# Kernel tuning notes

Measured on AMD Instinct MI355X. Metric: run time of the kernel, lower is better.

## Reference

```python
import jax, jax.numpy as jnp
import numpy as np

ALPHA = 0.2          # LeakyReLU negative slope
NEG = -9.0e15        # masking value from the torch code
B, N, F, O, H = 8, 1024, 256, 128, 8


def setup_inputs() -> dict:
    key = jax.random.key(0)
    ks = jax.random.split(key, 12)
    inputs = jax.random.normal(ks[0], (B, N, F), dtype=jnp.float32)
    adj = jax.random.randint(ks[1], (B, N, N), 0, 2, dtype=jnp.int32)
    mask = jnp.ones((B, N), dtype=jnp.float32)  # unused by forward, kept for signature fidelity
    s = 0.08
    # per-head GAT layers (stacked): W [H,F,O], attention vector a split into src/dst halves
    W_att = jax.random.normal(ks[2], (H, F, O), dtype=jnp.float32) * s
    a_src = jax.random.normal(ks[3], (H, O), dtype=jnp.float32) * s
    a_dst = jax.random.normal(ks[4], (H, O), dtype=jnp.float32) * s
    # output GAT layer: in = H*O, out = O
    W_out = jax.random.normal(ks[5], (H * O, O), dtype=jnp.float32) * s
    ao_src = jax.random.normal(ks[6], (O,), dtype=jnp.float32) * s
    ao_dst = jax.random.normal(ks[7], (O,), dtype=jnp.float32) * s
    # nn.Linear(H*O, O) and nn.Linear(O, O)
    lin_w = jax.random.normal(ks[8], (O, H * O), dtype=jnp.float32) * s
    lin_b = jax.random.normal(ks[9], (O,), dtype=jnp.float32) * s
    ln_w = jax.random.normal(ks[10], (O, O), dtype=jnp.float32) * s
    ln_b = jax.random.normal(ks[11], (O,), dtype=jnp.float32) * s
    return {"inputs": inputs, "adj": adj, "mask": mask, "W_att": W_att, "a_src": a_src,
            "a_dst": a_dst, "W_out": W_out, "ao_src": ao_src, "ao_dst": ao_dst,
            "lin_w": lin_w, "lin_b": lin_b, "ln_w": ln_w, "ln_b": ln_b}


def _gat_heads(x, adj, W, asrc, adst):
    # x: [B,N,Fin], W: [Hh,Fin,O]. e[b,h,i,j] = leakyrelu(h_i.a_src + h_j.a_dst)
    # (equal to torch's repeat/cat @ a without the O(N^2*2F) intermediate)
    h = jnp.einsum('bnf,hfo->bhno', x, W)
    s1 = jnp.einsum('bhno,ho->bhn', h, asrc)
    s2 = jnp.einsum('bhno,ho->bhn', h, adst)
    e = jax.nn.leaky_relu(s1[:, :, :, None] + s2[:, :, None, :], ALPHA)
    att = jax.nn.softmax(jnp.where(adj[:, None, :, :] > 0, e, NEG), axis=-1)
    return jnp.einsum('bhij,bhjo->bhio', att, h)  # [B,Hh,N,O]


def reference(inputs, adj, mask, W_att, a_src, a_dst, W_out, ao_src, ao_dst,
              lin_w, lin_b, ln_w, ln_b):
    b, n, _ = inputs.shape
    # layer 0: multi-head GAT, concat=True -> elu, then concat over heads
    hp = _gat_heads(inputs, adj, W_att, a_src, a_dst)              # [B,H,N,O]
    x = jax.nn.elu(hp).transpose(0, 2, 1, 3).reshape(b, n, -1)     # [B,N,H*O]
    # layer 1 (residual): linear(x) + out_att(x, adj) (concat=False, no elu)
    out = _gat_heads(x, adj, W_out[None], ao_src[None], ao_dst[None])[:, 0]  # [B,N,O]
    x = x @ lin_w.T + lin_b + out
    # final projection + relu
    return jax.nn.relu(x @ ln_w.T + ln_b)
```

## Files before the change

### kernel.cpp

```cpp
#include <hip/hip_runtime.h>


#define NN 1024
#define FF 256
#define OO 128
#define HH 8
#define HO 1024

typedef __attribute__((ext_vector_type(8))) short short8;
typedef __attribute__((ext_vector_type(4))) float floatx4;

__device__ __forceinline__ ushort f2b(float f) {
    union { float f; unsigned u; } v; v.f = f;
    unsigned r = v.u + 0x7FFFu + ((v.u >> 16) & 1u);
    return (ushort)(r >> 16);
}

__global__ __launch_bounds__(256) void pack_adj(
    const int* __restrict__ adj, unsigned long long* __restrict__ adjp)
{
    int w = blockIdx.x * 4 + (threadIdx.x >> 6);
    int lane = threadIdx.x & 63;
    const int* row = adj + (long)w * NN;
#pragma unroll
    for (int it = 0; it < 16; it++) {
        unsigned long long m = __ballot(row[it * 64 + lane] > 0);
        if (lane == 0) adjp[(long)w * 16 + it] = m;
    }
}

__global__ __launch_bounds__(256) void transpose_cvt(
    const float* __restrict__ src, ushort* __restrict__ dst, int R, int C)
{
    __shared__ float tile[64][65];
    int r0 = blockIdx.x * 64, c0 = blockIdx.y * 64;
    src += (long)blockIdx.z * R * C;
    dst += (long)blockIdx.z * R * C;
    int t = threadIdx.x;
    int lr = t >> 4, lc = (t & 15) * 4;
#pragma unroll
    for (int p = 0; p < 4; p++) {
        float4 v = *(const float4*)(src + (long)(r0 + p * 16 + lr) * C + c0 + lc);
        tile[p * 16 + lr][lc] = v.x; tile[p * 16 + lr][lc + 1] = v.y;
        tile[p * 16 + lr][lc + 2] = v.z; tile[p * 16 + lr][lc + 3] = v.w;
    }
    __syncthreads();
    int c = t >> 2, rq = (t & 3) * 16;
    union { ushort s[16]; uint4 q[2]; } u;
#pragma unroll
    for (int k = 0; k < 16; k++) u.s[k] = f2b(tile[rq + k][c]);
    uint4* dp = (uint4*)(dst + (long)(c0 + c) * R + r0 + rq);
    dp[0] = u.q[0]; dp[1] = u.q[1];
}

__global__ __launch_bounds__(256) void cvt_bf16_2(
    const float* __restrict__ s0, ushort* __restrict__ d0, long n0,
    const float* __restrict__ s1, ushort* __restrict__ d1)
{
    long i = ((long)blockIdx.x * 256 + threadIdx.x) * 8;
    const float* src; ushort* dst; long off;
    if (i < n0) { src = s0; dst = d0; off = i; }
    else        { src = s1; dst = d1; off = i - n0; }
    float4 v0 = *(const float4*)(src + off);
    float4 v1 = *(const float4*)(src + off + 4);
    union { ushort s[8]; uint4 q; } u;
    u.s[0] = f2b(v0.x); u.s[1] = f2b(v0.y); u.s[2] = f2b(v0.z); u.s[3] = f2b(v0.w);
    u.s[4] = f2b(v1.x); u.s[5] = f2b(v1.y); u.s[6] = f2b(v1.z); u.s[7] = f2b(v1.w);
    *(uint4*)(dst + off) = u.q;
}

__global__ __launch_bounds__(256) void gemmT(
    const ushort* __restrict__ AT, const float* __restrict__ Bf,
    ushort* __restrict__ Cb, float* __restrict__ s1, float* __restrict__ s2,
    const float* __restrict__ a1g, const float* __restrict__ a2g,
    int K, int Hh)
{
    int t = threadIdx.x;
    int wave = t >> 6, lane = t & 63;
    int quad = lane >> 4, l16 = lane & 15;
    int bh = blockIdx.y;
    int hh = bh % Hh, b = bh / Hh;
    int n0w = blockIdx.x * 64 + wave * 16;

    const ushort* A = AT + (long)hh * OO * K;
    const float* browf = Bf + ((long)b * NN + n0w + l16) * K;

    floatx4 acc[8];
    floatx4 zero = {0.f, 0.f, 0.f, 0.f};
#pragma unroll
    for (int mt = 0; mt < 8; mt++) acc[mt] = zero;

    for (int k0 = 0; k0 < K; k0 += 32) {
        int kb = k0 + quad * 8;
        float4 b0 = *(const float4*)(browf + kb);
        float4 b1 = *(const float4*)(browf + kb + 4);
        short8 bfr;
        bfr[0] = (short)f2b(b0.x); bfr[1] = (short)f2b(b0.y);
        bfr[2] = (short)f2b(b0.z); bfr[3] = (short)f2b(b0.w);
        bfr[4] = (short)f2b(b1.x); bfr[5] = (short)f2b(b1.y);
        bfr[6] = (short)f2b(b1.z); bfr[7] = (short)f2b(b1.w);
#pragma unroll
        for (int mt = 0; mt < 8; mt++) {
            short8 af = *(const short8*)(A + (long)(mt * 16 + l16) * K + kb);
            acc[mt] = __builtin_amdgcn_mfma_f32_16x16x32_bf16(af, bfr, acc[mt], 0, 0, 0);
        }
    }

    const float* a1 = a1g + hh * OO;
    const float* a2 = a2g + hh * OO;
    float sp1 = 0.f, sp2 = 0.f;
#pragma unroll
    for (int mt = 0; mt < 8; mt++) {
        float4 v1 = *(const float4*)(a1 + mt * 16 + quad * 4);
        float4 v2 = *(const float4*)(a2 + mt * 16 + quad * 4);
        sp1 += acc[mt][0] * v1.x + acc[mt][1] * v1.y + acc[mt][2] * v1.z + acc[mt][3] * v1.w;
        sp2 += acc[mt][0] * v2.x + acc[mt][1] * v2.y + acc[mt][2] * v2.z + acc[mt][3] * v2.w;
    }
    sp1 += __shfl_xor(sp1, 16); sp1 += __shfl_xor(sp1, 32);
    sp2 += __shfl_xor(sp2, 16); sp2 += __shfl_xor(sp2, 32);
    if (lane < 16) {
        s1[(long)bh * NN + n0w + l16] = sp1;
        s2[(long)bh * NN + n0w + l16] = sp2;
    }

    ushort* cb = Cb + (long)bh * OO * NN;
    int n = n0w + l16;
    int base = (n >> 3) * 1024 + (n & 7);
#pragma unroll
    for (int mt = 0; mt < 8; mt++) {
#pragma unroll
        for (int reg = 0; reg < 4; reg++) {
            int o = mt * 16 + quad * 4 + reg;
            cb[base + o * 8] = f2b(acc[mt][reg]);
        }
    }
}

__global__ __launch_bounds__(256) void gemmT_sk(
    const ushort* __restrict__ AT,
    const ushort* __restrict__ Bb,
    ushort* __restrict__ Cb,
    float* __restrict__ s1, float* __restrict__ s2,
    const float* __restrict__ a1g, const float* __restrict__ a2g)
{
    __shared__ float red[4 * 2304];
    int t = threadIdx.x;
    int wave = t >> 6, lane = t & 63;
    int quad = lane >> 4, l16 = lane & 15;
    int b = blockIdx.y;
    int n0 = blockIdx.x * 16;

    const ushort* brow = Bb + ((long)b * NN + n0 + l16) * HO;
    int kbase = wave * 256;

    floatx4 acc[8];
    floatx4 zero = {0.f, 0.f, 0.f, 0.f};
#pragma unroll
    for (int mt = 0; mt < 8; mt++) acc[mt] = zero;

    for (int k0 = 0; k0 < 256; k0 += 32) {
        int kb = kbase + k0 + quad * 8;
        short8 bfr = *(const short8*)(brow + kb);
#pragma unroll
        for (int mt = 0; mt < 8; mt++) {
            short8 af = *(const short8*)(AT + (long)(mt * 16 + l16) * HO + kb);
            acc[mt] = __builtin_amdgcn_mfma_f32_16x16x32_bf16(af, bfr, acc[mt], 0, 0, 0);
        }
    }

#pragma unroll
    for (int mt = 0; mt < 8; mt++)
#pragma unroll
        for (int reg = 0; reg < 4; reg++)
            red[wave * 2304 + (mt * 16 + quad * 4 + reg) * 18 + l16] = acc[mt][reg];
    __syncthreads();

    int nl = t & 15, g = t >> 4, o0 = g * 8;
    float s[8];
#pragma unroll
    for (int k = 0; k < 8; k++) {
        int idx = (o0 + k) * 18 + nl;
        s[k] = red[idx] + red[2304 + idx] + red[4608 + idx] + red[6912 + idx];
    }

    float p1 = 0.f, p2 = 0.f;
#pragma unroll
    for (int k = 0; k < 8; k++) {
        p1 += s[k] * a1g[o0 + k];
        p2 += s[k] * a2g[o0 + k];
    }

    ushort* cb = Cb + (long)b * OO * NN;
    int nglob = n0 + nl;
    int base = (nglob >> 3) * 1024 + (nglob & 7);
#pragma unroll
    for (int k = 0; k < 8; k++) cb[base + (o0 + k) * 8] = f2b(s[k]);

    __syncthreads();
    red[g * 16 + nl] = p1;
    red[256 + g * 16 + nl] = p2;
    __syncthreads();
    if (t < 16) {
        float q1 = 0.f, q2 = 0.f;
#pragma unroll
        for (int gg = 0; gg < 16; gg++) {
            q1 += red[gg * 16 + t];
            q2 += red[256 + gg * 16 + t];
        }
        s1[(long)b * NN + n0 + t] = q1;
        s2[(long)b * NN + n0 + t] = q2;
    }
}

template <int JS>
__global__ __launch_bounds__(256) void attn_mfma(
    const float* __restrict__ s1g, const float* __restrict__ s2g,
    const ushort* __restrict__ hTp, const uint* __restrict__ adjp,
    float* __restrict__ outf, ushort* __restrict__ outb,
    int Hh, int outStride, int doElu, int writeBf)
{
    extern __shared__ float smem_f[];
    float* s2s = smem_f;
    float* red = smem_f + NN;
    float* Lred = red + 8448;

    int t = threadIdx.x;
    int wave = t >> 6, lane = t & 63;
    int quad = lane >> 4, l16 = lane & 15;
    int bh = blockIdx.y;
    int hh = bh % Hh, b = bh / Hh;

    const float* s2r = s2g + (long)bh * NN;
    for (int j = t; j < NN; j += 256) s2s[j] = s2r[j];
    __syncthreads();

    const ushort* hT = hTp + (long)bh * OO * NN;
    const ushort* hbase = hT + quad * 1024 + l16 * 8;
    floatx4 zero = {0.f, 0.f, 0.f, 0.f};

    if (JS == 2) {
        int ig = wave >> 1, jh = wave & 1;
        int i0 = blockIdx.x * 64 + ig * 32;
        int j_lo = jh * (NN / 2), j_hi = j_lo + NN / 2;

        float s1a = s1g[(long)bh * NN + i0 + l16];
        float s1b = s1g[(long)bh * NN + i0 + 16 + l16];
        const uint* abA = adjp + ((long)b * NN + i0 + l16) * 32;
        const uint* abB = abA + 16 * 32;

        floatx4 acc0[8], acc1[8];
#pragma unroll
        for (int ot = 0; ot < 8; ot++) { acc0[ot] = zero; acc1[ot] = zero; }
        float Lp0 = 0.f, Lp1 = 0.f;

        for (int j0 = j_lo; j0 < j_hi; j0 += 32) {
            const ushort* hp = hbase + (j0 >> 3) * 1024;
            short8 bf[8];
#pragma unroll
            for (int ot = 0; ot < 8; ot++)
                bf[ot] = *(const short8*)(hp + ot * 128);
            uint mbA = (abA[j0 >> 5] >> (quad * 8)) & 0xffu;
            uint mbB = (abB[j0 >> 5] >> (quad * 8)) & 0xffu;
            int kb = j0 + quad * 8;
            float4 sA4 = *(const float4*)(s2s + kb);
            float4 sB4 = *(const float4*)(s2s + kb + 4);
            float se[8] = {sA4.x, sA4.y, sA4.z, sA4.w, sB4.x, sB4.y, sB4.z, sB4.w};
            short8 afA, afB;
#pragma unroll
            for (int e = 0; e < 8; e++) {
                float ea = s1a + se[e]; ea = fmaxf(ea, 0.2f * ea);
                float eb = s1b + se[e]; eb = fmaxf(eb, 0.2f * eb);
                union { float f; uint u; } wa, wb;
                wa.f = ((mbA >> e) & 1u) ? __expf(ea) : 0.f;
                wb.f = ((mbB >> e) & 1u) ? __expf(eb) : 0.f;
                wa.u &= 0xffff0000u; wb.u &= 0xffff0000u;
                afA[e] = (short)(wa.u >> 16);
                afB[e] = (short)(wb.u >> 16);
                Lp0 += wa.f; Lp1 += wb.f;
            }
#pragma unroll
            for (int ot = 0; ot < 8; ot++) {
                acc0[ot] = __builtin_amdgcn_mfma_f32_16x16x32_bf16(afA, bf[ot], acc0[ot], 0, 0, 0);
                acc1[ot] = __builtin_amdgcn_mfma_f32_16x16x32_bf16(afB, bf[ot], acc1[ot], 0, 0, 0);
            }
        }

        Lp0 += __shfl_xor(Lp0, 16); Lp0 += __shfl_xor(Lp0, 32);
        Lp1 += __shfl_xor(Lp1, 16); Lp1 += __shfl_xor(Lp1, 32);

        if (jh == 1) {
#pragma unroll
            for (int ot = 0; ot < 8; ot++)
#pragma unroll
                for (int reg = 0; reg < 4; reg++) {
                    red[(ig * 32 + quad * 4 + reg) * 132 + ot * 16 + l16] = acc0[ot][reg];
                    red[(ig * 32 + 16 + quad * 4 + reg) * 132 + ot * 16 + l16] = acc1[ot][reg];
                }
            if (lane < 16) {
                Lred[(ig * 2 + 0) * 16 + l16] = Lp0;
                Lred[(ig * 2 + 1) * 16 + l16] = Lp1;
            }
        }
        __syncthreads();
        if (jh == 0) {
            float r0 = 1.0f / (Lp0 + Lred[(ig * 2 + 0) * 16 + l16]);
            float r1 = 1.0f / (Lp1 + Lred[(ig * 2 + 1) * 16 + l16]);
#pragma unroll
            for (int tile = 0; tile < 2; tile++) {
                float rv = tile ? r1 : r0;
                floatx4* ac = tile ? acc1 : acc0;
#pragma unroll
                for (int reg = 0; reg < 4; reg++) {
                    float linv = __shfl(rv, quad * 4 + reg);
                    int rloc = ig * 32 + tile * 16 + quad * 4 + reg;
                    int row = blockIdx.x * 64 + rloc;
                    if (writeBf) {
                        ushort* orow = outb + (long)b * NN * outStride + hh * OO +
                                       (long)row * outStride + l16;
#pragma unroll
                        for (int ot = 0; ot < 8; ot++) {
                            float v = (ac[ot][reg] + red[rloc * 132 + ot * 16 + l16]) * linv;
                            if (doElu) v = (v > 0.f) ? v : (__expf(v) - 1.0f);
                            orow[ot * 16] = f2b(v);
                        }
                    } else {
                        float* orow = outf + (long)b * NN * outStride + hh * OO +
                                      (long)row * outStride + l16;
#pragma unroll
                        for (int ot = 0; ot < 8; ot++) {
                            float v = (ac[ot][reg] + red[rloc * 132 + ot * 16 + l16]) * linv;
                            if (doElu) v = (v > 0.f) ? v : (__expf(v) - 1.0f);
                            orow[ot * 16] = v;
                        }
                    }
                }
            }
        }
    } else {
        int i0 = blockIdx.x * 16;
        int j_lo = wave * (NN / 4), j_hi = j_lo + NN / 4;

        float s1a = s1g[(long)bh * NN + i0 + l16];
        const uint* abA = adjp + ((long)b * NN + i0 + l16) * 32;

        floatx4 acc[8];
#pragma unroll
        for (int ot = 0; ot < 8; ot++) acc[ot] = zero;
        float Lp = 0.f;

        for (int j0 = j_lo; j0 < j_hi; j0 += 32) {
            const ushort* hp = hbase + (j0 >> 3) * 1024;
            short8 bf[8];
#pragma unroll
            for (int ot = 0; ot < 8; ot++)
                bf[ot] = *(const short8*)(hp + ot * 128);
            uint mbA = (abA[j0 >> 5] >> (quad * 8)) & 0xffu;
            int kb = j0 + quad * 8;
            float4 sA4 = *(const float4*)(s2s + kb);
            float4 sB4 = *(const float4*)(s2s + kb + 4);
            float se[8] = {sA4.x, sA4.y, sA4.z, sA4.w, sB4.x, sB4.y, sB4.z, sB4.w};
            short8 afA;
#pragma unroll
            for (int e = 0; e < 8; e++) {
                float ea = s1a + se[e]; ea = fmaxf(ea, 0.2f * ea);
                union { float f; uint u; } wa;
                wa.f = ((mbA >> e) & 1u) ? __expf(ea) : 0.f;
                wa.u &= 0xffff0000u;
                afA[e] = (short)(wa.u >> 16);
                Lp += wa.f;
            }
#pragma unroll
            for (int ot = 0; ot < 8; ot++)
                acc[ot] = __builtin_amdgcn_mfma_f32_16x16x32_bf16(afA, bf[ot], acc[ot], 0, 0, 0);
        }

        Lp += __shfl_xor(Lp, 16); Lp += __shfl_xor(Lp, 32);
#pragma unroll
        for (int ot = 0; ot < 8; ot++)
#pragma unroll
            for (int reg = 0; reg < 4; reg++)
                red[(wave * 16 + quad * 4 + reg) * 132 + ot * 16 + l16] = acc[ot][reg];
        if (lane < 16) Lred[wave * 16 + l16] = Lp;
        __syncthreads();
        int row = t >> 4, c0 = (t & 15) * 8;
        float L = Lred[row] + Lred[16 + row] + Lred[32 + row] + Lred[48 + row];
        float rinv = 1.0f / L;
        int grow = i0 + row;
        float vv[8];
#pragma unroll
        for (int k = 0; k < 8; k++) {
            float s = red[row * 132 + c0 + k] + red[(16 + row) * 132 + c0 + k] +
                      red[(32 + row) * 132 + c0 + k] + red[(48 + row) * 132 + c0 + k];
            float v = s * rinv;
            if (doElu) v = (v > 0.f) ? v : (__expf(v) - 1.0f);
            vv[k] = v;
        }
        if (writeBf) {
            ushort* orow = outb + (long)b * NN * outStride + hh * OO +
                           (long)grow * outStride + c0;
#pragma unroll
            for (int k = 0; k < 8; k++) orow[k] = f2b(vv[k]);
        } else {
            float* orow = outf + (long)b * NN * outStride + hh * OO +
                          (long)grow * outStride + c0;
            *(float4*)orow = make_float4(vv[0], vv[1], vv[2], vv[3]);
            *(float4*)(orow + 4) = make_float4(vv[4], vv[5], vv[6], vv[7]);
        }
    }
}

__global__ __launch_bounds__(256) void final_mfma(
    const ushort* __restrict__ xb, const float* __restrict__ out2,
    const ushort* __restrict__ lwb, const float* __restrict__ lin_b,
    const ushort* __restrict__ nwb, const float* __restrict__ ln_b,
    float* __restrict__ out)
{
    __shared__ ushort ys[32][136];
    int t = threadIdx.x;
    int wave = t >> 6, lane = t & 63;
    int quad = lane >> 4, l16 = lane & 15;
    long row0 = (long)blockIdx.x * 32;
    int n0 = wave * 32;

    floatx4 zero = {0.f, 0.f, 0.f, 0.f};
    floatx4 acc[2][2];
#pragma unroll
    for (int mt = 0; mt < 2; mt++)
#pragma unroll
        for (int nt = 0; nt < 2; nt++) acc[mt][nt] = zero;

    for (int k0 = 0; k0 < HO; k0 += 32) {
        int kb = k0 + quad * 8;
        short8 a0 = *(const short8*)(xb + (row0 + l16) * HO + kb);
        short8 a1 = *(const short8*)(xb + (row0 + 16 + l16) * HO + kb);
        short8 b0 = *(const short8*)(lwb + (long)(n0 + l16) * HO + kb);
        short8 b1 = *(const short8*)(lwb + (long)(n0 + 16 + l16) * HO + kb);
        acc[0][0] = __builtin_amdgcn_mfma_f32_16x16x32_bf16(a0, b0, acc[0][0], 0, 0, 0);
        acc[0][1] = __builtin_amdgcn_mfma_f32_16x16x32_bf16(a0, b1, acc[0][1], 0, 0, 0);
        acc[1][0] = __builtin_amdgcn_mfma_f32_16x16x32_bf16(a1, b0, acc[1][0], 0, 0, 0);
        acc[1][1] = __builtin_amdgcn_mfma_f32_16x16x32_bf16(a1, b1, acc[1][1], 0, 0, 0);
    }

#pragma unroll
    for (int nt = 0; nt < 2; nt++) {
        int col = n0 + nt * 16 + l16;
        float lb = lin_b[col];
#pragma unroll
        for (int mt = 0; mt < 2; mt++) {
#pragma unroll
            for (int reg = 0; reg < 4; reg++) {
                int row = mt * 16 + quad * 4 + reg;
                float v = acc[mt][nt][reg] + lb + out2[(row0 + row) * OO + col];
                ys[row][col] = f2b(v);
            }
        }
    }
    __syncthreads();

    floatx4 acc2[2][2];
#pragma unroll
    for (int mt = 0; mt < 2; mt++)
#pragma unroll
        for (int nt = 0; nt < 2; nt++) acc2[mt][nt] = zero;

#pragma unroll
    for (int k0 = 0; k0 < OO; k0 += 32) {
        int kb = k0 + quad * 8;
        short8 a0 = *(const short8*)&ys[l16][kb];
        short8 a1 = *(const short8*)&ys[16 + l16][kb];
        short8 b0 = *(const short8*)(nwb + (long)(n0 + l16) * OO + kb);
        short8 b1 = *(const short8*)(nwb + (long)(n0 + 16 + l16) * OO + kb);
        acc2[0][0] = __builtin_amdgcn_mfma_f32_16x16x32_bf16(a0, b0, acc2[0][0], 0, 0, 0);
        acc2[0][1] = __builtin_amdgcn_mfma_f32_16x16x32_bf16(a0, b1, acc2[0][1], 0, 0, 0);
        acc2[1][0] = __builtin_amdgcn_mfma_f32_16x16x32_bf16(a1, b0, acc2[1][0], 0, 0, 0);
        acc2[1][1] = __builtin_amdgcn_mfma_f32_16x16x32_bf16(a1, b1, acc2[1][1], 0, 0, 0);
    }

#pragma unroll
    for (int nt = 0; nt < 2; nt++) {
        int col = n0 + nt * 16 + l16;
        float nb = ln_b[col];
#pragma unroll
        for (int mt = 0; mt < 2; mt++) {
#pragma unroll
            for (int reg = 0; reg < 4; reg++) {
                int row = mt * 16 + quad * 4 + reg;
                out[(row0 + row) * OO + col] = fmaxf(acc2[mt][nt][reg] + nb, 0.f);
            }
        }
    }
}

extern "C" void kernel_launch(void* const* d_in, const int* in_sizes, int n_in,
                              void* d_out, int out_size, void* d_ws, size_t ws_size,
                              hipStream_t stream)
{
    const float* inputs = (const float*)d_in[0];
    const int*   adj    = (const int*)d_in[1];
    const float* W_att  = (const float*)d_in[3];
    const float* a_src  = (const float*)d_in[4];
    const float* a_dst  = (const float*)d_in[5];
    const float* W_out  = (const float*)d_in[6];
    const float* ao_src = (const float*)d_in[7];
    const float* ao_dst = (const float*)d_in[8];
    const float* lin_w  = (const float*)d_in[9];
    const float* lin_b  = (const float*)d_in[10];
    const float* ln_w   = (const float*)d_in[11];
    const float* ln_b   = (const float*)d_in[12];
    float* out = (float*)d_out;

    float* ws   = (float*)d_ws;
    float* out2 = ws;
    float* s1   = ws + 1048576;
    float* s2   = ws + 1114112;
    float* s1o  = ws + 1179648;
    float* s2o  = ws + 1187840;
    ushort* ub      = (ushort*)(ws + 1196032);
    ushort* x_b     = ub;
    ushort* h_catTb = ub + 8388608;
    ushort* h2Tb    = ub + 16777216;
    ushort* W_attTb = ub + 17825792;
    ushort* W_outTb = ub + 18087936;
    ushort* lin_wb  = ub + 18219008;
    ushort* ln_wb   = ub + 18350080;
    unsigned long long* adjp = (unsigned long long*)(ub + 18366464);

    const int SH = (NN + 8448 + 64) * 4;

    pack_adj<<<2048, 256, 0, stream>>>(adj, adjp);
    transpose_cvt<<<dim3(4, 2, 8), 256, 0, stream>>>(W_att, W_attTb, FF, OO);
    transpose_cvt<<<dim3(16, 2, 1), 256, 0, stream>>>(W_out, W_outTb, HO, OO);
    cvt_bf16_2<<<72, 256, 0, stream>>>(lin_w, lin_wb, 131072L, ln_w, ln_wb);
    gemmT<<<dim3(16, 64), 256, 0, stream>>>(
        W_attTb, inputs, h_catTb, s1, s2, a_src, a_dst, FF, HH);
    attn_mfma<2><<<dim3(16, 64), 256, SH, stream>>>(
        s1, s2, h_catTb, (const uint*)adjp, (float*)nullptr, x_b, HH, HO, 1, 1);
    gemmT_sk<<<dim3(64, 8), 256, 0, stream>>>(
        W_outTb, x_b, h2Tb, s1o, s2o, ao_src, ao_dst);
    attn_mfma<4><<<dim3(64, 8), 256, SH, stream>>>(
        s1o, s2o, h2Tb, (const uint*)adjp, out2, (ushort*)nullptr, 1, OO, 0, 0);
    final_mfma<<<256, 256, 0, stream>>>(
        x_b, out2, lin_wb, lin_b, ln_wb, ln_b, out);
}
```

Measured before the change: 249.7 us.

## Pack weights into k-chunked bf16 layout and stage inputs in LDS for first GEMM

Replaces the three weight-conversion kernels with a single pack_weights kernel that writes all weights as bf16 in a k-chunk-major layout ([k/8][row][8]), so each MFMA fragment load across lanes is contiguous. The first projection GEMM now converts an input tile to bf16 once into shared memory instead of each of eight per-head blocks reconverting from fp32 global memory in the inner loop. The downstream GEMMs read the new packed layout. This removes two kernel launches and improves coalescing, at the cost of an extra LDS barrier and higher shared-memory use in gemmT0.

```diff
diff --git a/kernel.cpp b/kernel.cpp
--- a/kernel.cpp
+++ b/kernel.cpp
@@ -29,79 +29,92 @@
     }
 }
 
-__global__ __launch_bounds__(256) void transpose_cvt(
-    const float* __restrict__ src, ushort* __restrict__ dst, int R, int C)
-{
-    __shared__ float tile[64][65];
-    int r0 = blockIdx.x * 64, c0 = blockIdx.y * 64;
-    src += (long)blockIdx.z * R * C;
-    dst += (long)blockIdx.z * R * C;
-    int t = threadIdx.x;
-    int lr = t >> 4, lc = (t & 15) * 4;
-#pragma unroll
-    for (int p = 0; p < 4; p++) {
-        float4 v = *(const float4*)(src + (long)(r0 + p * 16 + lr) * C + c0 + lc);
-        tile[p * 16 + lr][lc] = v.x; tile[p * 16 + lr][lc + 1] = v.y;
-        tile[p * 16 + lr][lc + 2] = v.z; tile[p * 16 + lr][lc + 3] = v.w;
-    }
-    __syncthreads();
-    int c = t >> 2, rq = (t & 3) * 16;
-    union { ushort s[16]; uint4 q[2]; } u;
-#pragma unroll
-    for (int k = 0; k < 16; k++) u.s[k] = f2b(tile[rq + k][c]);
-    uint4* dp = (uint4*)(dst + (long)(c0 + c) * R + r0 + rq);
-    dp[0] = u.q[0]; dp[1] = u.q[1];
-}
-
-__global__ __launch_bounds__(256) void cvt_bf16_2(
-    const float* __restrict__ s0, ushort* __restrict__ d0, long n0,
-    const float* __restrict__ s1, ushort* __restrict__ d1)
-{
-    long i = ((long)blockIdx.x * 256 + threadIdx.x) * 8;
-    const float* src; ushort* dst; long off;
-    if (i < n0) { src = s0; dst = d0; off = i; }
-    else        { src = s1; dst = d1; off = i - n0; }
-    float4 v0 = *(const float4*)(src + off);
-    float4 v1 = *(const float4*)(src + off + 4);
+__global__ __launch_bounds__(256) void pack_weights(
+    const float* __restrict__ W_att, const float* __restrict__ W_out,
+    const float* __restrict__ lin_w, const float* __restrict__ ln_w,
+    ushort* __restrict__ WAp, ushort* __restrict__ WOp,
+    ushort* __restrict__ LWp, ushort* __restrict__ NWp)
+{
+    int tid = blockIdx.x * 256 + threadIdx.x;
+    float v[8];
+    ushort* dst;
+    if (tid < 32768) {
+        int h = tid >> 12, rem = tid & 4095, kc = rem >> 7, o = rem & 127;
+        const float* s = W_att + h * 32768;
+#pragma unroll
+        for (int i = 0; i < 8; i++) v[i] = s[(kc * 8 + i) * 128 + o];
+        dst = WAp + h * 32768 + kc * 1024 + o * 8;
+    } else if (tid < 49152) {
+        int t2 = tid - 32768;
+        int kc = t2 >> 7, o = t2 & 127;
+#pragma unroll
+        for (int i = 0; i < 8; i++) v[i] = W_out[(kc * 8 + i) * 128 + o];
+        dst = WOp + kc * 1024 + o * 8;
+    } else if (tid < 65536) {
+        int t3 = tid - 49152;
+        int kc = t3 >> 7, c = t3 & 127;
+        float4 a = *(const float4*)(lin_w + c * 1024 + kc * 8);
+        float4 bq = *(const float4*)(lin_w + c * 1024 + kc * 8 + 4);
+        v[0] = a.x; v[1] = a.y; v[2] = a.z; v[3] = a.w;
+        v[4] = bq.x; v[5] = bq.y; v[6] = bq.z; v[7] = bq.w;
+        dst = LWp + kc * 1024 + c * 8;
+    } else {
+        int t4 = tid - 65536;
+        int kc = t4 >> 7, c = t4 & 127;
+        float4 a = *(const float4*)(ln_w + c * 128 + kc * 8);
+        float4 bq = *(const float4*)(ln_w + c * 128 + kc * 8 + 4);
+        v[0] = a.x; v[1] = a.y; v[2] = a.z; v[3] = a.w;
+        v[4] = bq.x; v[5] = bq.y; v[6] = bq.z; v[7] = bq.w;
+        dst = NWp + kc * 1024 + c * 8;
+    }
     union { ushort s[8]; uint4 q; } u;
-    u.s[0] = f2b(v0.x); u.s[1] = f2b(v0.y); u.s[2] = f2b(v0.z); u.s[3] = f2b(v0.w);
-    u.s[4] = f2b(v1.x); u.s[5] = f2b(v1.y); u.s[6] = f2b(v1.z); u.s[7] = f2b(v1.w);
-    *(uint4*)(dst + off) = u.q;
-}
-
-__global__ __launch_bounds__(256) void gemmT(
-    const ushort* __restrict__ AT, const float* __restrict__ Bf,
+#pragma unroll
+    for (int i = 0; i < 8; i++) u.s[i] = f2b(v[i]);
+    *(uint4*)dst = u.q;
+}
+
+__global__ __launch_bounds__(256) void gemmT0(
+    const ushort* __restrict__ WAp, const float* __restrict__ inputs,
     ushort* __restrict__ Cb, float* __restrict__ s1, float* __restrict__ s2,
-    const float* __restrict__ a1g, const float* __restrict__ a2g,
-    int K, int Hh)
-{
+    const float* __restrict__ a1g, const float* __restrict__ a2g)
+{
+    __shared__ ushort Bs[32 * 520];
     int t = threadIdx.x;
     int wave = t >> 6, lane = t & 63;
     int quad = lane >> 4, l16 = lane & 15;
     int bh = blockIdx.y;
-    int hh = bh % Hh, b = bh / Hh;
-    int n0w = blockIdx.x * 64 + wave * 16;
-
-    const ushort* A = AT + (long)hh * OO * K;
-    const float* browf = Bf + ((long)b * NN + n0w + l16) * K;
-
+    int hh = bh & 7, b = bh >> 3;
+    int nblk = blockIdx.x * 64;
+    int n0w = nblk + wave * 16;
+
+    const float* binp = inputs + ((long)b * NN + nblk) * FF;
+#pragma unroll
+    for (int it = 0; it < 8; it++) {
+        int pid = it * 256 + t;
+        int kc = pid & 31, r = pid >> 5;
+        float4 va = *(const float4*)(binp + r * FF + kc * 8);
+        float4 vb = *(const float4*)(binp + r * FF + kc * 8 + 4);
+        union { ushort s[8]; uint4 q; } u;
+        u.s[0] = f2b(va.x); u.s[1] = f2b(va.y); u.s[2] = f2b(va.z); u.s[3] = f2b(va.w);
+        u.s[4] = f2b(vb.x); u.s[5] = f2b(vb.y); u.s[6] = f2b(vb.z); u.s[7] = f2b(vb.w);
+        *(uint4*)&Bs[kc * 520 + r * 8] = u.q;
+    }
+    __syncthreads();
+
+    const ushort* A = WAp + hh * 32768;
+    int nl = wave * 16 + l16;
     floatx4 acc[8];
     floatx4 zero = {0.f, 0.f, 0.f, 0.f};
 #pragma unroll
     for (int mt = 0; mt < 8; mt++) acc[mt] = zero;
 
-    for (int k0 = 0; k0 < K; k0 += 32) {
-        int kb = k0 + quad * 8;
-        float4 b0 = *(const float4*)(browf + kb);
-        float4 b1 = *(const float4*)(browf + kb + 4);
-        short8 bfr;
-        bfr[0] = (short)f2b(b0.x); bfr[1] = (short)f2b(b0.y);
-        bfr[2] = (short)f2b(b0.z); bfr[3] = (short)f2b(b0.w);
-        bfr[4] = (short)f2b(b1.x); bfr[5] = (short)f2b(b1.y);
-        bfr[6] = (short)f2b(b1.z); bfr[7] = (short)f2b(b1.w);
+#pragma unroll 2
+    for (int kc2 = 0; kc2 < 8; kc2++) {
+        int kc = kc2 * 4 + quad;
+        short8 bfr = *(const short8*)&Bs[kc * 520 + nl * 8];
 #pragma unroll
         for (int mt = 0; mt < 8; mt++) {
-            short8 af = *(const short8*)(A + (long)(mt * 16 + l16) * K + kb);
+            short8 af = *(const short8*)(A + kc * 1024 + (mt * 16 + l16) * 8);
             acc[mt] = __builtin_amdgcn_mfma_f32_16x16x32_bf16(af, bfr, acc[mt], 0, 0, 0);
         }
     }
@@ -137,7 +150,7 @@
 }
 
 __global__ __launch_bounds__(256) void gemmT_sk(
-    const ushort* __restrict__ AT,
+    const ushort* __restrict__ WOp,
     const ushort* __restrict__ Bb,
     ushort* __restrict__ Cb,
     float* __restrict__ s1, float* __restrict__ s2,
@@ -160,10 +173,11 @@
 
     for (int k0 = 0; k0 < 256; k0 += 32) {
         int kb = kbase + k0 + quad * 8;
+        int kch = kb >> 3;
         short8 bfr = *(const short8*)(brow + kb);
 #pragma unroll
         for (int mt = 0; mt < 8; mt++) {
-            short8 af = *(const short8*)(AT + (long)(mt * 16 + l16) * HO + kb);
+            short8 af = *(const short8*)(WOp + kch * 1024 + (mt * 16 + l16) * 8);
             acc[mt] = __builtin_amdgcn_mfma_f32_16x16x32_bf16(af, bfr, acc[mt], 0, 0, 0);
         }
     }
@@ -411,8 +425,8 @@
 
 __global__ __launch_bounds__(256) void final_mfma(
     const ushort* __restrict__ xb, const float* __restrict__ out2,
-    const ushort* __restrict__ lwb, const float* __restrict__ lin_b,
-    const ushort* __restrict__ nwb, const float* __restrict__ ln_b,
+    const ushort* __restrict__ LWp, const float* __restrict__ lin_b,
+    const ushort* __restrict__ NWp, const float* __restrict__ ln_b,
     float* __restrict__ out)
 {
     __shared__ ushort ys[32][136];
@@ -431,10 +445,11 @@
 
     for (int k0 = 0; k0 < HO; k0 += 32) {
         int kb = k0 + quad * 8;
+        int kch = kb >> 3;
         short8 a0 = *(const short8*)(xb + (row0 + l16) * HO + kb);
         short8 a1 = *(const short8*)(xb + (row0 + 16 + l16) * HO + kb);
-        short8 b0 = *(const short8*)(lwb + (long)(n0 + l16) * HO + kb);
-        short8 b1 = *(const short8*)(lwb + (long)(n0 + 16 + l16) * HO + kb);
+        short8 b0 = *(const short8*)(LWp + kch * 1024 + (n0 + l16) * 8);
+        short8 b1 = *(const short8*)(LWp + kch * 1024 + (n0 + 16 + l16) * 8);
         acc[0][0] = __builtin_amdgcn_mfma_f32_16x16x32_bf16(a0, b0, acc[0][0], 0, 0, 0);
         acc[0][1] = __builtin_amdgcn_mfma_f32_16x16x32_bf16(a0, b1, acc[0][1], 0, 0, 0);
         acc[1][0] = __builtin_amdgcn_mfma_f32_16x16x32_bf16(a1, b0, acc[1][0], 0, 0, 0);
@@ -466,10 +481,11 @@
 #pragma unroll
     for (int k0 = 0; k0 < OO; k0 += 32) {
         int kb = k0 + quad * 8;
+        int kch = kb >> 3;
         short8 a0 = *(const short8*)&ys[l16][kb];
         short8 a1 = *(const short8*)&ys[16 + l16][kb];
-        short8 b0 = *(const short8*)(nwb + (long)(n0 + l16) * OO + kb);
-        short8 b1 = *(const short8*)(nwb + (long)(n0 + 16 + l16) * OO + kb);
+        short8 b0 = *(const short8*)(NWp + kch * 1024 + (n0 + l16) * 8);
+        short8 b1 = *(const short8*)(NWp + kch * 1024 + (n0 + 16 + l16) * 8);
         acc2[0][0] = __builtin_amdgcn_mfma_f32_16x16x32_bf16(a0, b0, acc2[0][0], 0, 0, 0);
         acc2[0][1] = __builtin_amdgcn_mfma_f32_16x16x32_bf16(a0, b1, acc2[0][1], 0, 0, 0);
         acc2[1][0] = __builtin_amdgcn_mfma_f32_16x16x32_bf16(a1, b0, acc2[1][0], 0, 0, 0);
@@ -519,26 +535,25 @@
     ushort* x_b     = ub;
     ushort* h_catTb = ub + 8388608;
     ushort* h2Tb    = ub + 16777216;
-    ushort* W_attTb = ub + 17825792;
-    ushort* W_outTb = ub + 18087936;
-    ushort* lin_wb  = ub + 18219008;
-    ushort* ln_wb   = ub + 18350080;
+    ushort* WAp     = ub + 17825792;
+    ushort* WOp     = ub + 18087936;
+    ushort* LWp     = ub + 18219008;
+    ushort* NWp     = ub + 18350080;
     unsigned long long* adjp = (unsigned long long*)(ub + 18366464);
 
     const int SH = (NN + 8448 + 64) * 4;
 
     pack_adj<<<2048, 256, 0, stream>>>(adj, adjp);
-    transpose_cvt<<<dim3(4, 2, 8), 256, 0, stream>>>(W_att, W_attTb, FF, OO);
-    transpose_cvt<<<dim3(16, 2, 1), 256, 0, stream>>>(W_out, W_outTb, HO, OO);
-    cvt_bf16_2<<<72, 256, 0, stream>>>(lin_w, lin_wb, 131072L, ln_w, ln_wb);
-    gemmT<<<dim3(16, 64), 256, 0, stream>>>(
-        W_attTb, inputs, h_catTb, s1, s2, a_src, a_dst, FF, HH);
+    pack_weights<<<264, 256, 0, stream>>>(
+        W_att, W_out, lin_w, ln_w, WAp, WOp, LWp, NWp);
+    gemmT0<<<dim3(16, 64), 256, 0, stream>>>(
+        WAp, inputs, h_catTb, s1, s2, a_src, a_dst);
     attn_mfma<2><<<dim3(16, 64), 256, SH, stream>>>(
         s1, s2, h_catTb, (const uint*)adjp, (float*)nullptr, x_b, HH, HO, 1, 1);
     gemmT_sk<<<dim3(64, 8), 256, 0, stream>>>(
-        W_outTb, x_b, h2Tb, s1o, s2o, ao_src, ao_dst);
+        WOp, x_b, h2Tb, s1o, s2o, ao_src, ao_dst);
     attn_mfma<4><<<dim3(64, 8), 256, SH, stream>>>(
         s1o, s2o, h2Tb, (const uint*)adjp, out2, (ushort*)nullptr, 1, OO, 0, 0);
     final_mfma<<<256, 256, 0, stream>>>(
-        x_b, out2, lin_wb, lin_b, ln_wb, ln_b, out);
-}
+        x_b, out2, LWp, lin_b, NWp, ln_b, out);
+}
```

Measured after the change: 214.5 us. -14.1%, faster.
